# Kernel optimization log

Hardware: AMD Instinct MI355X
Metric: run time of the kernel (lower is better)

## Reference

```python
import jax, jax.numpy as jnp
import numpy as np

B, N, M = 8, 1024, 1024
DIM2 = 1280          # config.dim * 2
KIN = 1344           # esm_dim + cell_line_dim
H, DK = 8, 64        # heads, attn_dim_key
SCALE = DK ** -0.5


def setup_inputs() -> dict:
    key = jax.random.key(0)
    ks = jax.random.split(key, 7)
    rna_reps = jax.random.normal(ks[0], (B, N, DIM2), dtype=jnp.float32)
    protein_reps = jax.random.normal(ks[1], (B, M, KIN), dtype=jnp.float32)
    # learned params (Linear stores weight [out, in])
    Wq = jax.random.normal(ks[2], (H * DK, DIM2), dtype=jnp.float32) * (DIM2 ** -0.5)
    bq = jnp.zeros((H * DK,), dtype=jnp.float32)
    Wk = jax.random.normal(ks[3], (H * DK, KIN), dtype=jnp.float32) * (KIN ** -0.5)
    bk = jnp.zeros((H * DK,), dtype=jnp.float32)
    rel_bias = jax.random.normal(ks[4], (1, H, 1, DK), dtype=jnp.float32)
    return {"rna_reps": rna_reps, "protein_reps": protein_reps,
            "Wq": Wq, "bq": bq, "Wk": Wk, "bk": bk, "rel_bias": rel_bias}


def reference(rna_reps, protein_reps, Wq, bq, Wk, bk, rel_bias):
    b = rna_reps.shape[0]
    q = rna_reps @ Wq.T + bq           # [b, n, h*dk]
    k = protein_reps @ Wk.T + bk       # [b, m, h*dk]
    q = q.reshape(b, N, H, DK).transpose(0, 2, 1, 3)   # b h n d
    k = k.reshape(b, M, H, DK).transpose(0, 2, 1, 3)   # b h m d
    q = q * SCALE
    logits = jnp.einsum('bhid,bhjd->bhij', q + rel_bias, k)  # [b,h,n,m]
    out = jnp.mean(logits, axis=1)     # mean over heads -> [b,n,m]
    # dropout p=0.0 (eval) -> identity
    return out
```

## Files before the change

### kernel.cpp

```cpp
#include <hip/hip_runtime.h>
#include <hip/hip_bf16.h>


typedef __bf16 bf16x8 __attribute__((ext_vector_type(8)));
typedef float f32x4 __attribute__((ext_vector_type(4)));

__device__ inline bf16x8 cvt2(const f32x4 a, const f32x4 b) {
    bf16x8 r;
    r[0] = (__bf16)a[0]; r[1] = (__bf16)a[1]; r[2] = (__bf16)a[2]; r[3] = (__bf16)a[3];
    r[4] = (__bf16)b[0]; r[5] = (__bf16)b[1]; r[6] = (__bf16)b[2]; r[7] = (__bf16)b[3];
    return r;
}

__global__ __launch_bounds__(256, 2)
void proj_all(const float* __restrict__ rna,  const float* __restrict__ prot,
              const float* __restrict__ Wq,   const float* __restrict__ bq,
              const float* __restrict__ Wk,   const float* __restrict__ bk,
              const float* __restrict__ rb,
              __bf16* __restrict__ qout, __bf16* __restrict__ kout)
{
    __shared__ float As[128 * 64];
    __shared__ float Ws[128 * 64];

    const int bid = blockIdx.x;
    const int wg  = (bid & 7) * 64 + (bid >> 3);
    const bool isQ = wg < 256;
    const int lwg  = isQ ? wg : wg - 256;
    const int brow = (lwg >> 2) * 128;
    const int bcol = (lwg & 3) * 128;

    const float* A    = isQ ? rna : prot;
    const float* W    = isQ ? Wq  : Wk;
    const float* bias = isQ ? bq  : bk;
    __bf16*      out  = isQ ? qout : kout;
    const int    K    = isQ ? 1280 : 1344;

    const int tid  = threadIdx.x;
    const int lane = tid & 63;
    const int wid  = tid >> 6;
    const int wr   = wid >> 1;
    const int wc   = wid & 1;
    const int fr   = lane & 15;
    const int q4   = lane >> 4;

    const int lrow = lane >> 4;
    const int ciE  = (lane & 15) ^ (lrow << 1);
    const int ciO  = ciE ^ 1;
    const float* aBaseE = A + (size_t)(brow + wid * 32 + lrow) * K + ciE * 4;
    const float* aBaseO = A + (size_t)(brow + wid * 32 + lrow) * K + ciO * 4;
    const float* wBaseE = W + (size_t)(bcol + wid * 32 + lrow) * K + ciE * 4;
    const float* wBaseO = W + (size_t)(bcol + wid * 32 + lrow) * K + ciO * 4;

    const int rmask = ((fr & 3) << 1) | ((fr >> 2) & 1);

    f32x4 acc[4][4] = {};

    for (int k0 = 0; k0 < K; k0 += 64) {
        __syncthreads();
        #pragma unroll
        for (int i = 0; i < 8; ++i) {
            const float* sa = ((i & 1) ? aBaseO : aBaseE) + (size_t)(i * 4) * K + k0;
            const float* sw = ((i & 1) ? wBaseO : wBaseE) + (size_t)(i * 4) * K + k0;
            __builtin_amdgcn_global_load_lds(
                (const __attribute__((address_space(1))) void*)sa,
                (__attribute__((address_space(3))) void*)&As[(wid * 32 + i * 4) * 64], 16, 0, 0);
            __builtin_amdgcn_global_load_lds(
                (const __attribute__((address_space(1))) void*)sw,
                (__attribute__((address_space(3))) void*)&Ws[(wid * 32 + i * 4) * 64], 16, 0, 0);
        }
        __syncthreads();

        #pragma unroll
        for (int kk = 0; kk < 2; ++kk) {
            const int c0 = kk * 8 + 2 * q4;
            bf16x8 af[4], bw[4];
            #pragma unroll
            for (int m = 0; m < 4; ++m) {
                const float* rowp = &As[(wr * 64 + m * 16 + fr) * 64];
                f32x4 v0 = *(const f32x4*)(rowp + (((c0    ) ^ rmask) << 2));
                f32x4 v1 = *(const f32x4*)(rowp + (((c0 + 1) ^ rmask) << 2));
                af[m] = cvt2(v0, v1);
            }
            #pragma unroll
            for (int n = 0; n < 4; ++n) {
                const float* rowp = &Ws[(wc * 64 + n * 16 + fr) * 64];
                f32x4 v0 = *(const f32x4*)(rowp + (((c0    ) ^ rmask) << 2));
                f32x4 v1 = *(const f32x4*)(rowp + (((c0 + 1) ^ rmask) << 2));
                bw[n] = cvt2(v0, v1);
            }
            #pragma unroll
            for (int m = 0; m < 4; ++m)
                #pragma unroll
                for (int n = 0; n < 4; ++n)
                    acc[m][n] = __builtin_amdgcn_mfma_f32_16x16x32_bf16(af[m], bw[n], acc[m][n], 0, 0, 0);
        }
    }

    const int r0 = (lane >> 4) * 4;
    #pragma unroll
    for (int n = 0; n < 4; ++n) {
        const int c = bcol + wc * 64 + n * 16 + fr;
        const float bv = bias[c];
        const float rv = isQ ? rb[c] : 0.0f;
        #pragma unroll
        for (int m = 0; m < 4; ++m) {
            const int row = brow + wr * 64 + m * 16 + r0;
            #pragma unroll
            for (int j = 0; j < 4; ++j) {
                float v = acc[m][n][j] + bv;
                if (isQ) v = 0.125f * v + rv;
                out[(size_t)(row + j) * 512 + c] = (__bf16)v;
            }
        }
    }
}

__global__ __launch_bounds__(256, 2)
void attn_kernel(const __bf16* __restrict__ Q,
                 const __bf16* __restrict__ Kb,
                 float* __restrict__ out)
{
    __shared__ __bf16 As[128 * 64];
    __shared__ __bf16 Bs[128 * 64];

    const int tid  = threadIdx.x;
    const int lane = tid & 63;
    const int wid  = tid >> 6;
    const int wr   = wid >> 1;
    const int wc   = wid & 1;
    const int b    = blockIdx.z;
    const int brow = blockIdx.y * 128;
    const int bcol = blockIdx.x * 128;

    const __bf16* Qb = Q  + (size_t)b * 1024 * 512;
    const __bf16* Kp = Kb + (size_t)b * 1024 * 512;

    const int fr = lane & 15;
    const int q4 = lane >> 4;

    f32x4 acc[4][4] = {};

    const int lr3 = lane >> 3;
    const int m3  = ((lr3 & 3) << 1) | ((lr3 >> 2) & 1);
    const int scol = ((lane & 7) ^ m3) * 8;
    const int rmask = ((fr & 3) << 1) | ((fr >> 2) & 1);

    for (int k0 = 0; k0 < 512; k0 += 64) {
        __syncthreads();
        #pragma unroll
        for (int i = 0; i < 4; ++i) {
            const int rbase = wid * 32 + i * 8;
            const __bf16* sa = Qb + (size_t)(brow + rbase + lr3) * 512 + k0 + scol;
            const __bf16* sb = Kp + (size_t)(bcol + rbase + lr3) * 512 + k0 + scol;
            __builtin_amdgcn_global_load_lds(
                (const __attribute__((address_space(1))) void*)sa,
                (__attribute__((address_space(3))) void*)&As[rbase * 64], 16, 0, 0);
            __builtin_amdgcn_global_load_lds(
                (const __attribute__((address_space(1))) void*)sb,
                (__attribute__((address_space(3))) void*)&Bs[rbase * 64], 16, 0, 0);
        }
        __syncthreads();

        #pragma unroll
        for (int kk = 0; kk < 2; ++kk) {
            const int ci = kk * 4 + q4;
            bf16x8 af[4], bf_[4];
            #pragma unroll
            for (int m = 0; m < 4; ++m)
                af[m] = *(const bf16x8*)(&As[(wr * 64 + m * 16 + fr) * 64 + ((ci ^ rmask) << 3)]);
            #pragma unroll
            for (int n = 0; n < 4; ++n)
                bf_[n] = *(const bf16x8*)(&Bs[(wc * 64 + n * 16 + fr) * 64 + ((ci ^ rmask) << 3)]);
            #pragma unroll
            for (int m = 0; m < 4; ++m)
                #pragma unroll
                for (int n = 0; n < 4; ++n)
                    acc[m][n] = __builtin_amdgcn_mfma_f32_16x16x32_bf16(af[m], bf_[n], acc[m][n], 0, 0, 0);
        }
    }

    float* op = out + (size_t)b * 1024 * 1024;
    const int r0 = (lane >> 4) * 4;
    #pragma unroll
    for (int n = 0; n < 4; ++n) {
        const int col = bcol + wc * 64 + n * 16 + fr;
        #pragma unroll
        for (int m = 0; m < 4; ++m) {
            const int row = brow + wr * 64 + m * 16 + r0;
            #pragma unroll
            for (int j = 0; j < 4; ++j)
                op[(size_t)(row + j) * 1024 + col] = 0.125f * acc[m][n][j];
        }
    }
}

extern "C" void kernel_launch(void* const* d_in, const int* in_sizes, int n_in,
                              void* d_out, int out_size, void* d_ws, size_t ws_size,
                              hipStream_t stream) {
    const float* rna  = (const float*)d_in[0];
    const float* prot = (const float*)d_in[1];
    const float* Wq   = (const float*)d_in[2];
    const float* bq   = (const float*)d_in[3];
    const float* Wk   = (const float*)d_in[4];
    const float* bk   = (const float*)d_in[5];
    const float* rb   = (const float*)d_in[6];

    __bf16* qws = (__bf16*)d_ws;
    __bf16* kws = qws + (size_t)8192 * 512;

    proj_all<<<dim3(512), dim3(256), 0, stream>>>(rna, prot, Wq, bq, Wk, bk, rb, qws, kws);
    attn_kernel<<<dim3(8, 8, 8), dim3(256), 0, stream>>>(qws, kws, (float*)d_out);
}
```

Baseline: 61.71 us.

## Register-prefetch projection tiles, convert to bf16 once, double-buffer LDS

The projection kernel no longer DMAs fp32 tiles straight into LDS. Each thread now loads the next K-tile into registers while the current one is used, converts it to bf16 once, and stores it into a double-buffered, swizzled bf16 LDS tile. This halves LDS footprint and read traffic, removes repeated fp32->bf16 conversion in the MFMA loop, and overlaps global loads with compute. In exchange it uses more registers (64 prefetch floats per thread), which may limit occupancy, and it drops the asynchronous global_load_lds path.

Measured after the change: 62.08 us. Within noise of the previous version (+0.6%).

```diff
diff --git a/kernel.cpp b/kernel.cpp
--- a/kernel.cpp
+++ b/kernel.cpp
@@ -3,12 +3,13 @@
 
 
 typedef __bf16 bf16x8 __attribute__((ext_vector_type(8)));
+typedef __bf16 bf16x4 __attribute__((ext_vector_type(4)));
 typedef float f32x4 __attribute__((ext_vector_type(4)));
 
-__device__ inline bf16x8 cvt2(const f32x4 a, const f32x4 b) {
-    bf16x8 r;
-    r[0] = (__bf16)a[0]; r[1] = (__bf16)a[1]; r[2] = (__bf16)a[2]; r[3] = (__bf16)a[3];
-    r[4] = (__bf16)b[0]; r[5] = (__bf16)b[1]; r[6] = (__bf16)b[2]; r[7] = (__bf16)b[3];
+__device__ inline bf16x4 cvt4(const f32x4 a) {
+    bf16x4 r;
+    r[0] = (__bf16)a[0]; r[1] = (__bf16)a[1];
+    r[2] = (__bf16)a[2]; r[3] = (__bf16)a[3];
     return r;
 }
 
@@ -19,8 +20,8 @@
               const float* __restrict__ rb,
               __bf16* __restrict__ qout, __bf16* __restrict__ kout)
 {
-    __shared__ float As[128 * 64];
-    __shared__ float Ws[128 * 64];
+    __shared__ __bf16 AS[2][128 * 64];
+    __shared__ __bf16 WS[2][128 * 64];
 
     const int bid = blockIdx.x;
     const int wg  = (bid & 7) * 64 + (bid >> 3);
@@ -34,6 +35,7 @@
     const float* bias = isQ ? bq  : bk;
     __bf16*      out  = isQ ? qout : kout;
     const int    K    = isQ ? 1280 : 1344;
+    const int    nt   = K >> 6;
 
     const int tid  = threadIdx.x;
     const int lane = tid & 63;
@@ -43,51 +45,53 @@
     const int fr   = lane & 15;
     const int q4   = lane >> 4;
 
-    const int lrow = lane >> 4;
-    const int ciE  = (lane & 15) ^ (lrow << 1);
-    const int ciO  = ciE ^ 1;
-    const float* aBaseE = A + (size_t)(brow + wid * 32 + lrow) * K + ciE * 4;
-    const float* aBaseO = A + (size_t)(brow + wid * 32 + lrow) * K + ciO * 4;
-    const float* wBaseE = W + (size_t)(bcol + wid * 32 + lrow) * K + ciE * 4;
-    const float* wBaseO = W + (size_t)(bcol + wid * 32 + lrow) * K + ciO * 4;
+    const int rloc = wid * 32 + q4;
+    const float* aGlob = A + (size_t)(brow + rloc) * K + fr * 4;
+    const float* wGlob = W + (size_t)(bcol + rloc) * K + fr * 4;
+    const int lb = rloc * 128 + (((fr >> 1) ^ (q4 << 1)) << 4) + (lane & 1) * 8;
 
     const int rmask = ((fr & 3) << 1) | ((fr >> 2) & 1);
 
     f32x4 acc[4][4] = {};
-
-    for (int k0 = 0; k0 < K; k0 += 64) {
+    f32x4 ra[8], rw[8];
+
+    #pragma unroll
+    for (int i = 0; i < 8; ++i) {
+        ra[i] = *(const f32x4*)(aGlob + (size_t)(i * 4) * K);
+        rw[i] = *(const f32x4*)(wGlob + (size_t)(i * 4) * K);
+    }
+
+    for (int t = 0; t < nt; ++t) {
+        char* as = (char*)AS[t & 1];
+        char* ws = (char*)WS[t & 1];
         __syncthreads();
         #pragma unroll
         for (int i = 0; i < 8; ++i) {
-            const float* sa = ((i & 1) ? aBaseO : aBaseE) + (size_t)(i * 4) * K + k0;
-            const float* sw = ((i & 1) ? wBaseO : wBaseE) + (size_t)(i * 4) * K + k0;
-            __builtin_amdgcn_global_load_lds(
-                (const __attribute__((address_space(1))) void*)sa,
-                (__attribute__((address_space(3))) void*)&As[(wid * 32 + i * 4) * 64], 16, 0, 0);
-            __builtin_amdgcn_global_load_lds(
-                (const __attribute__((address_space(1))) void*)sw,
-                (__attribute__((address_space(3))) void*)&Ws[(wid * 32 + i * 4) * 64], 16, 0, 0);
-        }
+            *(bf16x4*)(as + ((lb ^ ((i & 1) << 4)) + i * 512)) = cvt4(ra[i]);
+            *(bf16x4*)(ws + ((lb ^ ((i & 1) << 4)) + i * 512)) = cvt4(rw[i]);
+        }
+        if (t + 1 < nt) {
+            const int k0n = (t + 1) * 64;
+            #pragma unroll
+            for (int i = 0; i < 8; ++i) {
+                ra[i] = *(const f32x4*)(aGlob + (size_t)(i * 4) * K + k0n);
+                rw[i] = *(const f32x4*)(wGlob + (size_t)(i * 4) * K + k0n);
+            }
+        }
+        __builtin_amdgcn_sched_barrier(0);
         __syncthreads();
 
         #pragma unroll
         for (int kk = 0; kk < 2; ++kk) {
-            const int c0 = kk * 8 + 2 * q4;
             bf16x8 af[4], bw[4];
             #pragma unroll
-            for (int m = 0; m < 4; ++m) {
-                const float* rowp = &As[(wr * 64 + m * 16 + fr) * 64];
-                f32x4 v0 = *(const f32x4*)(rowp + (((c0    ) ^ rmask) << 2));
-                f32x4 v1 = *(const f32x4*)(rowp + (((c0 + 1) ^ rmask) << 2));
-                af[m] = cvt2(v0, v1);
-            }
-            #pragma unroll
-            for (int n = 0; n < 4; ++n) {
-                const float* rowp = &Ws[(wc * 64 + n * 16 + fr) * 64];
-                f32x4 v0 = *(const f32x4*)(rowp + (((c0    ) ^ rmask) << 2));
-                f32x4 v1 = *(const f32x4*)(rowp + (((c0 + 1) ^ rmask) << 2));
-                bw[n] = cvt2(v0, v1);
-            }
+            for (int m = 0; m < 4; ++m)
+                af[m] = *(const bf16x8*)(as + (wr * 64 + m * 16 + fr) * 128
+                                            + (((kk * 4 + q4) ^ rmask) << 4));
+            #pragma unroll
+            for (int n = 0; n < 4; ++n)
+                bw[n] = *(const bf16x8*)(ws + (wc * 64 + n * 16 + fr) * 128
+                                            + (((kk * 4 + q4) ^ rmask) << 4));
             #pragma unroll
             for (int m = 0; m < 4; ++m)
                 #pragma unroll
```

## Pre-convert weights to swizzled bf16 and retile projection GEMM to 64x256

Applied to the files above, without the earlier changes.

Adds a small kernel that converts Wq/Wk to bf16 once per call, writing them in a pre-swizzled layout so the projection kernel can load weight tiles straight into LDS without converting them in the inner loop. The projection kernel now uses 512-thread blocks with 64x256 output tiles. Activation reads per tile drop to a quarter of the columns re-read, and weight traffic halves in bytes. The cost is an extra launch plus a weight write/read round trip through the workspace.

Result: slower. 63.67 us (+3.2%).

```diff
diff --git a/kernel.cpp b/kernel.cpp
--- a/kernel.cpp
+++ b/kernel.cpp
@@ -12,99 +12,108 @@
     return r;
 }
 
-__global__ __launch_bounds__(256, 2)
+#define GLDS(src, dst) __builtin_amdgcn_global_load_lds( \
+    (const __attribute__((address_space(1))) void*)(src), \
+    (__attribute__((address_space(3))) void*)(dst), 16, 0, 0)
+
+__global__ __launch_bounds__(256)
+void wcvt(const float* __restrict__ Wq, const float* __restrict__ Wk,
+          __bf16* __restrict__ wqb, __bf16* __restrict__ wkb)
+{
+    const int id = blockIdx.x * 256 + threadIdx.x;
+    const int NQ = 512 * 160;
+    const float* src; __bf16* dst; int row, p, K;
+    if (id < NQ) { row = id / 160; p = id - row * 160; K = 1280; src = Wq; dst = wqb; }
+    else { const int t = id - NQ; row = t / 168; p = t - row * 168; K = 1344; src = Wk; dst = wkb; }
+    const int m3 = ((row & 3) << 1) | ((row >> 2) & 1);
+    const int c  = (p & ~7) | ((p & 7) ^ m3);
+    const f32x4 v0 = *(const f32x4*)(src + (size_t)row * K + c * 8);
+    const f32x4 v1 = *(const f32x4*)(src + (size_t)row * K + c * 8 + 4);
+    *(bf16x8*)(dst + (size_t)row * K + p * 8) = cvt2(v0, v1);
+}
+
+__global__ __launch_bounds__(512, 4)
 void proj_all(const float* __restrict__ rna,  const float* __restrict__ prot,
-              const float* __restrict__ Wq,   const float* __restrict__ bq,
-              const float* __restrict__ Wk,   const float* __restrict__ bk,
+              const __bf16* __restrict__ wqb, const __bf16* __restrict__ wkb,
+              const float* __restrict__ bq,   const float* __restrict__ bk,
               const float* __restrict__ rb,
               __bf16* __restrict__ qout, __bf16* __restrict__ kout)
 {
-    __shared__ float As[128 * 64];
-    __shared__ float Ws[128 * 64];
+    __shared__ float  As[64 * 64];
+    __shared__ __bf16 Ws[256 * 64];
 
     const int bid = blockIdx.x;
     const int wg  = (bid & 7) * 64 + (bid >> 3);
     const bool isQ = wg < 256;
     const int lwg  = isQ ? wg : wg - 256;
-    const int brow = (lwg >> 2) * 128;
-    const int bcol = (lwg & 3) * 128;
-
-    const float* A    = isQ ? rna : prot;
-    const float* W    = isQ ? Wq  : Wk;
-    const float* bias = isQ ? bq  : bk;
-    __bf16*      out  = isQ ? qout : kout;
-    const int    K    = isQ ? 1280 : 1344;
+    const int brow = (lwg >> 1) * 64;
+    const int bcol = (lwg & 1) * 256;
+
+    const float*  A    = isQ ? rna : prot;
+    const __bf16* Wb   = isQ ? wqb : wkb;
+    const float*  bias = isQ ? bq  : bk;
+    __bf16*       out  = isQ ? qout : kout;
+    const int     K    = isQ ? 1280 : 1344;
 
     const int tid  = threadIdx.x;
     const int lane = tid & 63;
     const int wid  = tid >> 6;
-    const int wr   = wid >> 1;
-    const int wc   = wid & 1;
     const int fr   = lane & 15;
     const int q4   = lane >> 4;
 
     const int lrow = lane >> 4;
-    const int ciE  = (lane & 15) ^ (lrow << 1);
-    const int ciO  = ciE ^ 1;
-    const float* aBaseE = A + (size_t)(brow + wid * 32 + lrow) * K + ciE * 4;
-    const float* aBaseO = A + (size_t)(brow + wid * 32 + lrow) * K + ciO * 4;
-    const float* wBaseE = W + (size_t)(bcol + wid * 32 + lrow) * K + ciE * 4;
-    const float* wBaseO = W + (size_t)(bcol + wid * 32 + lrow) * K + ciO * 4;
+    const int ciA  = (lane & 15) ^ (lrow << 1);
+    const float* aG0 = A + (size_t)(brow + wid * 8 + 0 + lrow) * K + ciA * 4;
+    const float* aG1 = A + (size_t)(brow + wid * 8 + 4 + lrow) * K + (ciA ^ 1) * 4;
+
+    const __bf16* wG = Wb + (size_t)(bcol + wid * 32 + (lane >> 3)) * K + (lane & 7) * 8;
 
     const int rmask = ((fr & 3) << 1) | ((fr >> 2) & 1);
 
-    f32x4 acc[4][4] = {};
+    f32x4 acc[4][2] = {};
 
     for (int k0 = 0; k0 < K; k0 += 64) {
         __syncthreads();
-        #pragma unroll
-        for (int i = 0; i < 8; ++i) {
-            const float* sa = ((i & 1) ? aBaseO : aBaseE) + (size_t)(i * 4) * K + k0;
-            const float* sw = ((i & 1) ? wBaseO : wBaseE) + (size_t)(i * 4) * K + k0;
-            __builtin_amdgcn_global_load_lds(
-                (const __attribute__((address_space(1))) void*)sa,
-                (__attribute__((address_space(3))) void*)&As[(wid * 32 + i * 4) * 64], 16, 0, 0);
-            __builtin_amdgcn_global_load_lds(
-                (const __attribute__((address_space(1))) void*)sw,
-                (__attribute__((address_space(3))) void*)&Ws[(wid * 32 + i * 4) * 64], 16, 0, 0);
-        }
+        GLDS(aG0 + k0, &As[wid * 512]);
+        GLDS(aG1 + k0, &As[wid * 512 + 256]);
+        #pragma unroll
+        for (int j = 0; j < 4; ++j)
+            GLDS(wG + (size_t)(j * 8) * K + k0, &Ws[(wid * 32 + j * 8) * 64]);
         __syncthreads();
 
         #pragma unroll
         for (int kk = 0; kk < 2; ++kk) {
             const int c0 = kk * 8 + 2 * q4;
-            bf16x8 af[4], bw[4];
+            const int cw = kk * 4 + q4;
+            bf16x8 af[4], bw[2];
             #pragma unroll
             for (int m = 0; m < 4; ++m) {
-                const float* rowp = &As[(wr * 64 + m * 16 + fr) * 64];
-                f32x4 v0 = *(const f32x4*)(rowp + (((c0    ) ^ rmask) << 2));
-                f32x4 v1 = *(const f32x4*)(rowp + (((c0 + 1) ^ rmask) << 2));
-                af[m] = cvt2(v0, v1);
+                const float* rp = &As[(m * 16 + fr) * 64];
+                f32x4 u0 = *(const f32x4*)(rp + (((c0    ) ^ rmask) << 2));
+                f32x4 u1 = *(const f32x4*)(rp + (((c0 + 1) ^ rmask) << 2));
+                af[m] = cvt2(u0, u1);
             }
             #pragma unroll
-            for (int n = 0; n < 4; ++n) {
-                const float* rowp = &Ws[(wc * 64 + n * 16 + fr) * 64];
-                f32x4 v0 = *(const f32x4*)(rowp + (((c0    ) ^ rmask) << 2));
-                f32x4 v1 = *(const f32x4*)(rowp + (((c0 + 1) ^ rmask) << 2));
-                bw[n] = cvt2(v0, v1);
-            }
+            for (int n = 0; n < 2; ++n)
+                bw[n] = *(const bf16x8*)(&Ws[(wid * 32 + n * 16 + fr) * 64
+                                             + ((cw ^ rmask) << 3)]);
             #pragma unroll
             for (int m = 0; m < 4; ++m)
                 #pragma unroll
-                for (int n = 0; n < 4; ++n)
+                for (int n = 0; n < 2; ++n)
                     acc[m][n] = __builtin_amdgcn_mfma_f32_16x16x32_bf16(af[m], bw[n], acc[m][n], 0, 0, 0);
         }
     }
 
-    const int r0 = (lane >> 4) * 4;
+    const int r0 = q4 * 4;
     #pragma unroll
-    for (int n = 0; n < 4; ++n) {
-        const int c = bcol + wc * 64 + n * 16 + fr;
+    for (int n = 0; n < 2; ++n) {
+        const int c = bcol + wid * 32 + n * 16 + fr;
         const float bv = bias[c];
         const float rv = isQ ? rb[c] : 0.0f;
         #pragma unroll
         for (int m = 0; m < 4; ++m) {
-            const int row = brow + wr * 64 + m * 16 + r0;
+            const int row = brow + m * 16 + r0;
             #pragma unroll
             for (int j = 0; j < 4; ++j) {
                 float v = acc[m][n][j] + bv;
@@ -150,14 +159,8 @@
         #pragma unroll
         for (int i = 0; i < 4; ++i) {
             const int rbase = wid * 32 + i * 8;
-            const __bf16* sa = Qb + (size_t)(brow + rbase + lr3) * 512 + k0 + scol;
-            const __bf16* sb = Kp + (size_t)(bcol + rbase + lr3) * 512 + k0 + scol;
-            __builtin_amdgcn_global_load_lds(
-                (const __attribute__((address_space(1))) void*)sa,
-                (__attribute__((address_space(3))) void*)&As[rbase * 64], 16, 0, 0);
-            __builtin_amdgcn_global_load_lds(
-                (const __attribute__((address_space(1))) void*)sb,
-                (__attribute__((address_space(3))) void*)&Bs[rbase * 64], 16, 0, 0);
+            GLDS(Qb + (size_t)(brow + rbase + lr3) * 512 + k0 + scol, &As[rbase * 64]);
+            GLDS(Kp + (size_t)(bcol + rbase + lr3) * 512 + k0 + scol, &Bs[rbase * 64]);
         }
         __syncthreads();
 
@@ -207,7 +210,10 @@
 
     __bf16* qws = (__bf16*)d_ws;
     __bf16* kws = qws + (size_t)8192 * 512;
-
-    proj_all<<<dim3(512), dim3(256), 0, stream>>>(rna, prot, Wq, bq, Wk, bk, rb, qws, kws);
+    __bf16* wqb = kws + (size_t)8192 * 512;
+    __bf16* wkb = wqb + (size_t)512 * 1280;
+
+    wcvt<<<dim3(656), dim3(256), 0, stream>>>(Wq, Wk, wqb, wkb);
+    proj_all<<<dim3(512), dim3(512), 0, stream>>>(rna, prot, wqb, wkb, bq, bk, rb, qws, kws);
     attn_kernel<<<dim3(8, 8, 8), dim3(256), 0, stream>>>(qws, kws, (float*)d_out);
 }
```
